# Performance work log

Measured on AMD Instinct MI355X. Metric: run time of the kernel, lower is better.

## Reference

```python
import jax, jax.numpy as jnp
import numpy as np

DIM = 256
HEADS = 8
HEAD_DIM = DIM // HEADS
WS = (2, 8, 8)  # window size (t, h, w)
N = WS[0] * WS[1] * WS[2]  # 128 tokens per window
SCALE = HEAD_DIM ** -0.5
MLP_HIDDEN = int(DIM * 2.0)
EPS = 1e-5

# static relative-position index table [N, N]
def _rel_pos_index():
    coords = np.stack(np.meshgrid(np.arange(WS[0]), np.arange(WS[1]), np.arange(WS[2]), indexing='ij'))
    cf = coords.reshape(3, -1)
    rel = cf[:, :, None] - cf[:, None, :]
    rel = rel.transpose(1, 2, 0).copy()
    rel[..., 0] += WS[0] - 1
    rel[..., 1] += WS[1] - 1
    rel[..., 2] += WS[2] - 1
    rel[..., 0] *= (2 * WS[1] - 1) * (2 * WS[2] - 1)
    rel[..., 1] *= (2 * WS[2] - 1)
    return rel.sum(-1)

REL_IDX = jnp.asarray(_rel_pos_index())  # [N, N] int
TABLE_SIZE = (2 * WS[0] - 1) * (2 * WS[1] - 1) * (2 * WS[2] - 1)  # 675


def layernorm(x, g, b):
    m = jnp.mean(x, axis=-1, keepdims=True)
    var = jnp.mean(jnp.square(x - m), axis=-1, keepdims=True)
    return (x - m) * jax.lax.rsqrt(var + EPS) * g + b


def window_partition(x):
    B, T, H, W, C = x.shape
    x = x.reshape(B, T // WS[0], WS[0], H // WS[1], WS[1], W // WS[2], WS[2], C)
    x = x.transpose(0, 1, 3, 5, 2, 4, 6, 7)
    return x.reshape(-1, N, C)


def window_reverse(wins, B, T, H, W):
    C = wins.shape[-1]
    x = wins.reshape(B, T // WS[0], H // WS[1], W // WS[2], WS[0], WS[1], WS[2], C)
    x = x.transpose(0, 1, 4, 2, 5, 3, 6, 7)
    return x.reshape(B, T, H, W, C)


def setup_inputs() -> dict:
    key = jax.random.key(0)
    ks = jax.random.split(key, 20)
    B, T, H, W = 2, 8, 64, 64
    f = lambda k, s, sc=0.02: jax.random.normal(k, s, dtype=jnp.float32) * sc
    return {
        'q': jax.random.normal(ks[0], (B, T, H, W, DIM), dtype=jnp.float32),
        'k': jax.random.normal(ks[1], (B, T, H, W, DIM), dtype=jnp.float32),
        'v': jax.random.normal(ks[2], (B, T, H, W, DIM), dtype=jnp.float32),
        'gq': jnp.ones((DIM,), jnp.float32), 'bq': jnp.zeros((DIM,), jnp.float32),
        'gk': jnp.ones((DIM,), jnp.float32), 'bk': jnp.zeros((DIM,), jnp.float32),
        'gv': jnp.ones((DIM,), jnp.float32), 'bv': jnp.zeros((DIM,), jnp.float32),
        'bias_table': f(ks[3], (TABLE_SIZE, HEADS)),
        'proj_w': f(ks[4], (DIM, DIM)), 'proj_b': jnp.zeros((DIM,), jnp.float32),
        'g2': jnp.ones((DIM,), jnp.float32), 'b2': jnp.zeros((DIM,), jnp.float32),
        'mw1': f(ks[5], (MLP_HIDDEN, DIM)), 'mb1': jnp.zeros((MLP_HIDDEN,), jnp.float32),
        'mw2': f(ks[6], (DIM, MLP_HIDDEN)), 'mb2': jnp.zeros((DIM,), jnp.float32),
    }


def reference(q, k, v, gq, bq, gk, bk, gv, bv, bias_table, proj_w, proj_b, g2, b2, mw1, mb1, mw2, mb2):
    B, T, H, W, C = q.shape
    shortcut = v
    qn = layernorm(q, gq, bq)
    kn = layernorm(k, gk, bk)
    vn = layernorm(v, gv, bv)
    # (dims divisible by window -> no padding needed)
    qw = window_partition(qn)  # [B_, N, C]
    kw = window_partition(kn)
    vw = window_partition(vn)
    B_ = qw.shape[0]
    to_heads = lambda t: t.reshape(B_, N, HEADS, HEAD_DIM).transpose(0, 2, 1, 3)  # [B_, h, N, d]
    qh, kh, vh = to_heads(qw), to_heads(kw), to_heads(vw)
    attn = jnp.einsum('bhnd,bhmd->bhnm', qh * SCALE, kh)
    bias = bias_table[REL_IDX]  # [N, N, heads]
    attn = attn + bias.transpose(2, 0, 1)[None]
    attn = jax.nn.softmax(attn, axis=-1)
    out = jnp.einsum('bhnm,bhmd->bhnd', attn, vh)
    out = out.transpose(0, 2, 1, 3).reshape(B_, N, C)
    out = out @ proj_w.T + proj_b
    x = window_reverse(out, B, T, H, W)
    x = shortcut + x
    h1 = layernorm(x, g2, b2)
    h1 = jax.nn.gelu(h1 @ mw1.T + mb1, approximate=False)
    x = x + (h1 @ mw2.T + mb2)
    return x
```

## Files before the change

kernel.cpp:

```cpp
#include <hip/hip_runtime.h>
#include <math.h>


typedef __attribute__((ext_vector_type(8))) short short8;
typedef __attribute__((ext_vector_type(4))) short shortx4;
typedef __attribute__((ext_vector_type(4))) float floatx4;

#define MFMA16(a, b, c) __builtin_amdgcn_mfma_f32_16x16x32_bf16((a), (b), (c), 0, 0, 0)
#define ATT_SCALE 0.17677669529663689f

__device__ __forceinline__ short f2bf(float f) {
  unsigned u = __float_as_uint(f);
  u += 0x7fffu + ((u >> 16) & 1u);
  return (short)(u >> 16);
}
__device__ __forceinline__ float bf2f(short s) {
  return __uint_as_float(((unsigned)(unsigned short)s) << 16);
}

__global__ void cvt_kernel(const float* __restrict__ src, short* __restrict__ dst, int n) {
  int i = blockIdx.x * 256 + threadIdx.x;
  if (i < n) dst[i] = f2bf(src[i]);
}

__global__ void biasprep_kernel(const float* __restrict__ table, short* __restrict__ biasPb) {
  int idx = blockIdx.x * 256 + threadIdx.x;
  int h = idx >> 14;
  int n = (idx >> 7) & 127;
  int lr = (idx >> 3) & 15;
  int c = idx & 7;
  int m = 16 * c + lr;
  int t1 = n >> 6, h1 = (n >> 3) & 7, w1 = n & 7;
  int t2 = m >> 6, h2 = (m >> 3) & 7, w2 = m & 7;
  int ridx = (t1 - t2 + 1) * 225 + (h1 - h2 + 7) * 15 + (w1 - w2 + 7);
  biasPb[idx] = f2bf(table[ridx * 8 + h]);
}

__global__ __launch_bounds__(256) void ln_qkv_kernel(
    const float* __restrict__ q, const float* __restrict__ k, const float* __restrict__ v,
    const float* __restrict__ gq, const float* __restrict__ bq,
    const float* __restrict__ gk, const float* __restrict__ bk,
    const float* __restrict__ gv, const float* __restrict__ bv,
    short* __restrict__ qw, short* __restrict__ kw, short* __restrict__ vw) {
  const int wv = threadIdx.x >> 6, l = threadIdx.x & 63;
  const int tok = blockIdx.x * 4 + wv;
  const int which = blockIdx.y;
  const float* src = (which == 0) ? q : ((which == 1) ? k : v);
  const float* gg  = (which == 0) ? gq : ((which == 1) ? gk : gv);
  const float* bb  = (which == 0) ? bq : ((which == 1) ? bk : bv);
  short* dst       = (which == 0) ? qw : ((which == 1) ? kw : vw);

  float4 xv = *(const float4*)(src + (size_t)tok * 256 + l * 4);
  float s1 = xv.x + xv.y + xv.z + xv.w;
  float s2 = xv.x * xv.x + xv.y * xv.y + xv.z * xv.z + xv.w * xv.w;
#pragma unroll
  for (int off = 1; off < 64; off <<= 1) {
    s1 += __shfl_xor(s1, off);
    s2 += __shfl_xor(s2, off);
  }
  float mean = s1 * (1.0f / 256.0f);
  float var = s2 * (1.0f / 256.0f) - mean * mean;
  float inv = rsqrtf(var + 1e-5f);

  int b_ = tok >> 15, rem = tok & 32767;
  int t = rem >> 12, hh = (rem >> 6) & 63, ww = rem & 63;
  int wi = ((b_ * 4 + (t >> 1)) * 8 + (hh >> 3)) * 8 + (ww >> 3);
  int n = ((t & 1) << 6) | ((hh & 7) << 3) | (ww & 7);

  float4 g4 = *(const float4*)(gg + l * 4);
  float4 b4 = *(const float4*)(bb + l * 4);
  shortx4 o;
  o[0] = f2bf((xv.x - mean) * inv * g4.x + b4.x);
  o[1] = f2bf((xv.y - mean) * inv * g4.y + b4.y);
  o[2] = f2bf((xv.z - mean) * inv * g4.z + b4.z);
  o[3] = f2bf((xv.w - mean) * inv * g4.w + b4.w);
  *(shortx4*)(dst + ((size_t)wi * 128 + n) * 256 + l * 4) = o;
}

__global__ __launch_bounds__(256, 4) void attn_kernel(
    const short* __restrict__ qw, const short* __restrict__ kw, const short* __restrict__ vw,
    const short* __restrict__ biasPb, short* __restrict__ ao) {
  __shared__ union SU {
    struct { short Qs[128][40]; short Ks[128][40]; } qk;
    short Ps[128 * 128];
  } su;
  __shared__ short Vt[32 * 128];

  const int wi = blockIdx.x, h = blockIdx.y, tid = threadIdx.x;
  const size_t base = (size_t)wi * 128 * 256 + h * 32;

#pragma unroll
  for (int i = 0; i < 2; ++i) {
    int idx = tid + 256 * i;
    int m = idx >> 2, c = idx & 3;
    *(short8*)&su.qk.Qs[m][c * 8] = *(const short8*)(qw + base + (size_t)m * 256 + c * 8);
    *(short8*)&su.qk.Ks[m][c * 8] = *(const short8*)(kw + base + (size_t)m * 256 + c * 8);
    short8 vv = *(const short8*)(vw + base + (size_t)m * 256 + c * 8);
#pragma unroll
    for (int e = 0; e < 8; ++e) {
      int d = c * 8 + e;
      Vt[d * 128 + (((m >> 3) ^ (d & 7)) << 3) + (m & 7)] = vv[e];
    }
  }
  __syncthreads();

  const int wvv = tid >> 6, l = tid & 63, lr = l & 15, g = l >> 4;
  const floatx4 zf = {0.f, 0.f, 0.f, 0.f};

  short8 aq0 = *(const short8*)&su.qk.Qs[32 * wvv + lr][g * 8];
  short8 aq1 = *(const short8*)&su.qk.Qs[32 * wvv + 16 + lr][g * 8];

  floatx4 s[2][8];
#pragma unroll
  for (int c = 0; c < 8; ++c) {
    short8 bk8 = *(const short8*)&su.qk.Ks[16 * c + lr][g * 8];
    s[0][c] = MFMA16(aq0, bk8, zf);
    s[1][c] = MFMA16(aq1, bk8, zf);
  }
  __syncthreads();

  const int lr7 = lr & 7;
#pragma unroll
  for (int r = 0; r < 2; ++r) {
#pragma unroll
    for (int j = 0; j < 4; ++j) {
      int n = 32 * wvv + 16 * r + 4 * g + j;
      short8 bv8 = *(const short8*)(biasPb + ((size_t)(h * 128 + n) * 16 + lr) * 8);
      float mx = -1e30f;
#pragma unroll
      for (int c = 0; c < 8; ++c) {
        float val = s[r][c][j] * ATT_SCALE + bf2f(bv8[c]);
        s[r][c][j] = val;
        mx = fmaxf(mx, val);
      }
#pragma unroll
      for (int off = 1; off < 16; off <<= 1) mx = fmaxf(mx, __shfl_xor(mx, off));
      float sum = 0.f;
#pragma unroll
      for (int c = 0; c < 8; ++c) {
        float e = __expf(s[r][c][j] - mx);
        s[r][c][j] = e;
        sum += e;
      }
#pragma unroll
      for (int off = 1; off < 16; off <<= 1) sum += __shfl_xor(sum, off);
      float invs = 1.0f / sum;
      int n7 = n & 7;
#pragma unroll
      for (int c = 0; c < 8; ++c) {
        int col = 16 * c + lr;
        su.Ps[n * 128 + (((col >> 3) ^ n7) << 3) + (col & 7)] = f2bf(s[r][c][j] * invs);
      }
    }
  }

  floatx4 o00 = zf, o01 = zf, o10 = zf, o11 = zf;
  const int ra0 = 32 * wvv + lr, ra1 = ra0 + 16;
#pragma unroll
  for (int ks = 0; ks < 4; ++ks) {
    int ulog = ks * 4 + g;
    short8 pa0 = *(const short8*)&su.Ps[ra0 * 128 + ((ulog ^ (ra0 & 7)) << 3)];
    short8 pa1 = *(const short8*)&su.Ps[ra1 * 128 + ((ulog ^ (ra1 & 7)) << 3)];
    short8 vb0 = *(const short8*)&Vt[lr * 128 + ((ulog ^ lr7) << 3)];
    short8 vb1 = *(const short8*)&Vt[(16 + lr) * 128 + ((ulog ^ lr7) << 3)];
    o00 = MFMA16(pa0, vb0, o00);
    o01 = MFMA16(pa0, vb1, o01);
    o10 = MFMA16(pa1, vb0, o10);
    o11 = MFMA16(pa1, vb1, o11);
  }
#pragma unroll
  for (int j = 0; j < 4; ++j) {
    int n0 = 32 * wvv + 4 * g + j;
    int n1 = n0 + 16;
    size_t rb0 = ((size_t)wi * 128 + n0) * 256 + h * 32;
    size_t rb1 = ((size_t)wi * 128 + n1) * 256 + h * 32;
    ao[rb0 + lr] = f2bf(o00[j]);
    ao[rb0 + 16 + lr] = f2bf(o01[j]);
    ao[rb1 + lr] = f2bf(o10[j]);
    ao[rb1 + 16 + lr] = f2bf(o11[j]);
  }
}

__global__ __launch_bounds__(512, 2) void projln_kernel(
    const short* __restrict__ ao, const short* __restrict__ wp,
    const float* __restrict__ proj_b, const float* __restrict__ vin,
    const float* __restrict__ g2, const float* __restrict__ b2,
    short* __restrict__ xbf, short* __restrict__ xln) {
  __shared__ short WS[256 * 256];

  const int tid = threadIdx.x;
  const int w = tid >> 6, l = tid & 63, lr = l & 15, g = l >> 4;
  const floatx4 zf = {0.f, 0.f, 0.f, 0.f};

#pragma unroll
  for (int c = 0; c < 16; ++c) {
    int idx = tid * 16 + c;
    int r = idx >> 5, u = idx & 31;
    short8 vv = *(const short8*)(wp + (size_t)r * 256 + u * 8);
    *(short8*)&WS[r * 256 + ((u ^ (r & 7)) << 3)] = vv;
  }

  const int rowbase = blockIdx.x * 256 + w * 32;
  short8 a[2][8];
#pragma unroll
  for (int mt = 0; mt < 2; ++mt)
#pragma unroll
    for (int s = 0; s < 8; ++s)
      a[mt][s] = *(const short8*)(ao + (size_t)(rowbase + mt * 16 + lr) * 256 + s * 32 + g * 8);

  __syncthreads();

  floatx4 acc[2][16];
#pragma unroll
  for (int mt = 0; mt < 2; ++mt)
#pragma unroll
    for (int ct = 0; ct < 16; ++ct) acc[mt][ct] = zf;

#pragma unroll
  for (int s = 0; s < 8; ++s) {
#pragma unroll
    for (int ct = 0; ct < 16; ++ct) {
      int rb = ct * 16 + lr;
      short8 b = *(const short8*)&WS[rb * 256 + (((s * 4 + g) ^ (rb & 7)) << 3)];
      acc[0][ct] = MFMA16(a[0][s], b, acc[0][ct]);
      acc[1][ct] = MFMA16(a[1][s], b, acc[1][ct]);
    }
  }

  float pb[16], g2v[16], b2v[16];
#pragma unroll
  for (int ct = 0; ct < 16; ++ct) {
    int col = ct * 16 + lr;
    pb[ct] = proj_b[col];
    g2v[ct] = g2[col];
    b2v[ct] = b2[col];
  }
#pragma unroll
  for (int mt = 0; mt < 2; ++mt) {
#pragma unroll
    for (int j = 0; j < 4; ++j) {
      int wrow = rowbase + mt * 16 + 4 * g + j;
      int wi = wrow >> 7, n = wrow & 127;
      int wb = wi & 7, hb = (wi >> 3) & 7, tt = (wi >> 6) & 3, b_ = wi >> 8;
      int t = tt * 2 + (n >> 6), hh = hb * 8 + ((n >> 3) & 7), ww2 = wb * 8 + (n & 7);
      size_t sidx = ((size_t)(b_ * 8 + t) * 64 + hh) * 64 + ww2;
      float xv[16], s1 = 0.f, s2 = 0.f;
#pragma unroll
      for (int ct = 0; ct < 16; ++ct) {
        float val = acc[mt][ct][j] + pb[ct] + vin[sidx * 256 + ct * 16 + lr];
        xv[ct] = val;
        s1 += val;
        s2 += val * val;
      }
#pragma unroll
      for (int off = 1; off < 16; off <<= 1) {
        s1 += __shfl_xor(s1, off);
        s2 += __shfl_xor(s2, off);
      }
      float mean = s1 * (1.0f / 256.0f);
      float var = s2 * (1.0f / 256.0f) - mean * mean;
      float inv = rsqrtf(var + 1e-5f);
#pragma unroll
      for (int ct = 0; ct < 16; ++ct) {
        int col = ct * 16 + lr;
        xbf[(size_t)wrow * 256 + col] = f2bf(xv[ct]);
        xln[(size_t)wrow * 256 + col] = f2bf((xv[ct] - mean) * inv * g2v[ct] + b2v[ct]);
      }
    }
  }
}

__global__ __launch_bounds__(512, 2) void mlp1_kernel(
    const short* __restrict__ xln, const short* __restrict__ w1,
    const float* __restrict__ mb1, short* __restrict__ h1) {
  __shared__ short WS[256 * 256];

  const int tid = threadIdx.x;
  const int w = tid >> 6, l = tid & 63, lr = l & 15, g = l >> 4;
  const int half = blockIdx.y;
  const floatx4 zf = {0.f, 0.f, 0.f, 0.f};
  const short* w1h = w1 + (size_t)half * 256 * 256;

#pragma unroll
  for (int c = 0; c < 16; ++c) {
    int idx = tid * 16 + c;
    int r = idx >> 5, u = idx & 31;
    short8 vv = *(const short8*)(w1h + (size_t)r * 256 + u * 8);
    *(short8*)&WS[r * 256 + ((u ^ (r & 7)) << 3)] = vv;
  }

  const int rowbase = blockIdx.x * 256 + w * 32;
  short8 a[2][8];
#pragma unroll
  for (int mt = 0; mt < 2; ++mt)
#pragma unroll
    for (int s = 0; s < 8; ++s)
      a[mt][s] = *(const short8*)(xln + (size_t)(rowbase + mt * 16 + lr) * 256 + s * 32 + g * 8);

  __syncthreads();

  floatx4 acc[2][16];
#pragma unroll
  for (int mt = 0; mt < 2; ++mt)
#pragma unroll
    for (int ct = 0; ct < 16; ++ct) acc[mt][ct] = zf;

#pragma unroll
  for (int s = 0; s < 8; ++s) {
#pragma unroll
    for (int ct = 0; ct < 16; ++ct) {
      int rb = ct * 16 + lr;
      short8 b = *(const short8*)&WS[rb * 256 + (((s * 4 + g) ^ (rb & 7)) << 3)];
      acc[0][ct] = MFMA16(a[0][s], b, acc[0][ct]);
      acc[1][ct] = MFMA16(a[1][s], b, acc[1][ct]);
    }
  }

  float bias[16];
#pragma unroll
  for (int ct = 0; ct < 16; ++ct) bias[ct] = mb1[half * 256 + ct * 16 + lr];
#pragma unroll
  for (int mt = 0; mt < 2; ++mt) {
#pragma unroll
    for (int j = 0; j < 4; ++j) {
      int wrow = rowbase + mt * 16 + 4 * g + j;
#pragma unroll
      for (int ct = 0; ct < 16; ++ct) {
        float xv = acc[mt][ct][j] + bias[ct];
        float yy = 1.5957691216057308f * (xv + 0.044715f * xv * xv * xv);
        float sg = 1.0f / (1.0f + __expf(-yy));
        h1[(size_t)wrow * 512 + half * 256 + ct * 16 + lr] = f2bf(xv * sg);
      }
    }
  }
}

__global__ __launch_bounds__(512, 2) void mlp2_kernel(
    const short* __restrict__ h1, const short* __restrict__ w2,
    const float* __restrict__ mb2, const short* __restrict__ xbf,
    float* __restrict__ out) {
  __shared__ short WS[128 * 512];

  const int tid = threadIdx.x;
  const int w = tid >> 6, l = tid & 63, lr = l & 15, g = l >> 4;
  const int half = blockIdx.y;
  const floatx4 zf = {0.f, 0.f, 0.f, 0.f};
  const short* w2h = w2 + (size_t)half * 128 * 512;

#pragma unroll
  for (int c = 0; c < 16; ++c) {
    int idx = tid * 16 + c;
    int r = idx >> 6, u = idx & 63;
    short8 vv = *(const short8*)(w2h + (size_t)r * 512 + u * 8);
    *(short8*)&WS[r * 512 + ((u ^ (r & 7)) << 3)] = vv;
  }
  __syncthreads();

  const int rowbase = blockIdx.x * 256 + w * 32;
  floatx4 acc[2][8];
#pragma unroll
  for (int mt = 0; mt < 2; ++mt)
#pragma unroll
    for (int ct = 0; ct < 8; ++ct) acc[mt][ct] = zf;

#pragma unroll
  for (int hk = 0; hk < 2; ++hk) {
    short8 a[2][8];
#pragma unroll
    for (int mt = 0; mt < 2; ++mt)
#pragma unroll
      for (int s = 0; s < 8; ++s)
        a[mt][s] = *(const short8*)(h1 + (size_t)(rowbase + mt * 16 + lr) * 512 +
                                    hk * 256 + s * 32 + g * 8);
#pragma unroll
    for (int s = 0; s < 8; ++s) {
      int S = hk * 8 + s;
#pragma unroll
      for (int ct = 0; ct < 8; ++ct) {
        int rb = ct * 16 + lr;
        short8 b = *(const short8*)&WS[rb * 512 + (((S * 4 + g) ^ (rb & 7)) << 3)];
        acc[0][ct] = MFMA16(a[0][s], b, acc[0][ct]);
        acc[1][ct] = MFMA16(a[1][s], b, acc[1][ct]);
      }
    }
  }

  float bias[8];
#pragma unroll
  for (int ct = 0; ct < 8; ++ct) bias[ct] = mb2[half * 128 + ct * 16 + lr];
#pragma unroll
  for (int mt = 0; mt < 2; ++mt) {
#pragma unroll
    for (int j = 0; j < 4; ++j) {
      int wrow = rowbase + mt * 16 + 4 * g + j;
      int wi = wrow >> 7, n = wrow & 127;
      int wb = wi & 7, hb = (wi >> 3) & 7, tt = (wi >> 6) & 3, b_ = wi >> 8;
      int t = tt * 2 + (n >> 6), hh = hb * 8 + ((n >> 3) & 7), ww2 = wb * 8 + (n & 7);
      size_t sidx = ((size_t)(b_ * 8 + t) * 64 + hh) * 64 + ww2;
#pragma unroll
      for (int ct = 0; ct < 8; ++ct) {
        int col = half * 128 + ct * 16 + lr;
        out[sidx * 256 + col] =
            bf2f(xbf[(size_t)wrow * 256 + col]) + acc[mt][ct][j] + bias[ct];
      }
    }
  }
}

extern "C" void kernel_launch(void* const* d_in, const int* in_sizes, int n_in,
                              void* d_out, int out_size, void* d_ws, size_t ws_size,
                              hipStream_t stream) {
  const float* q = (const float*)d_in[0];
  const float* k = (const float*)d_in[1];
  const float* v = (const float*)d_in[2];
  const float* gq = (const float*)d_in[3];
  const float* bq = (const float*)d_in[4];
  const float* gk = (const float*)d_in[5];
  const float* bk = (const float*)d_in[6];
  const float* gv = (const float*)d_in[7];
  const float* bv = (const float*)d_in[8];
  const float* bias_table = (const float*)d_in[9];
  const float* proj_w = (const float*)d_in[10];
  const float* proj_b = (const float*)d_in[11];
  const float* g2 = (const float*)d_in[12];
  const float* b2 = (const float*)d_in[13];
  const float* mw1 = (const float*)d_in[14];
  const float* mb1 = (const float*)d_in[15];
  const float* mw2 = (const float*)d_in[16];
  const float* mb2 = (const float*)d_in[17];

  char* ws = (char*)d_ws;
  short* qw = (short*)(ws + 0);
  short* kw = (short*)(ws + 33554432);
  short* vw = (short*)(ws + 67108864);
  short* ao = (short*)(ws + 100663296);
  short* xln = (short*)(ws + 0);
  short* xbf = (short*)(ws + 33554432);
  short* h1 = (short*)(ws + 67108864);
  short* wp = (short*)(ws + 167772160);
  short* w1 = (short*)(ws + 167903232);
  short* w2 = (short*)(ws + 168165376);
  short* biasPb = (short*)(ws + 168427520);

  cvt_kernel<<<256, 256, 0, stream>>>(proj_w, wp, 65536);
  cvt_kernel<<<512, 256, 0, stream>>>(mw1, w1, 131072);
  cvt_kernel<<<512, 256, 0, stream>>>(mw2, w2, 131072);
  biasprep_kernel<<<512, 256, 0, stream>>>(bias_table, biasPb);

  ln_qkv_kernel<<<dim3(16384, 3), 256, 0, stream>>>(q, k, v, gq, bq, gk, bk, gv, bv, qw, kw, vw);

  attn_kernel<<<dim3(512, 8), 256, 0, stream>>>(qw, kw, vw, biasPb, ao);

  projln_kernel<<<256, 512, 0, stream>>>(ao, wp, proj_b, v, g2, b2, xbf, xln);

  mlp1_kernel<<<dim3(256, 2), 512, 0, stream>>>(xln, w1, mb1, h1);

  mlp2_kernel<<<dim3(256, 2), 512, 0, stream>>>(h1, w2, mb2, xbf, (float*)d_out);
}
```

Before: 256.5 us.

## Write attention output in spatial order and transpose MFMA operands for vectorized epilogues

The attention kernel now scatters its output directly into spatial (B,T,H,W) token order, so the projection and MLP kernels index tokens linearly instead of recomputing window-reverse addresses. The three GEMM kernels swap MFMA operands so each lane holds four consecutive output columns for one token, which allows float4 and short4 vector loads and stores in the epilogues. They also stage weights into LDS in two K-halves, halving shared memory, and launch twice as many 128-row blocks with higher occupancy bounds. The cost is scattered writes in the attention epilogue, an extra barrier per GEMM, and weight tiles reloaded by more blocks.

```diff
diff --git a/kernel.cpp b/kernel.cpp
--- a/kernel.cpp
+++ b/kernel.cpp
@@ -168,12 +168,15 @@
     o10 = MFMA16(pa1, vb0, o10);
     o11 = MFMA16(pa1, vb1, o11);
   }
+  const int wbx = wi & 7, hbx = (wi >> 3) & 7, ttx = (wi >> 6) & 3, bbx = wi >> 8;
 #pragma unroll
   for (int j = 0; j < 4; ++j) {
     int n0 = 32 * wvv + 4 * g + j;
     int n1 = n0 + 16;
-    size_t rb0 = ((size_t)wi * 128 + n0) * 256 + h * 32;
-    size_t rb1 = ((size_t)wi * 128 + n1) * 256 + h * 32;
+    int t0 = ttx * 2 + (n0 >> 6), hh0 = hbx * 8 + ((n0 >> 3) & 7), ww0 = wbx * 8 + (n0 & 7);
+    int t1 = ttx * 2 + (n1 >> 6), hh1 = hbx * 8 + ((n1 >> 3) & 7), ww1 = wbx * 8 + (n1 & 7);
+    size_t rb0 = (((size_t)(bbx * 8 + t0) * 64 + hh0) * 64 + ww0) * 256 + h * 32;
+    size_t rb1 = (((size_t)(bbx * 8 + t1) * 64 + hh1) * 64 + ww1) * 256 + h * 32;
     ao[rb0 + lr] = f2bf(o00[j]);
     ao[rb0 + 16 + lr] = f2bf(o01[j]);
     ao[rb1 + lr] = f2bf(o10[j]);
@@ -181,229 +184,191 @@
   }
 }
 
-__global__ __launch_bounds__(512, 2) void projln_kernel(
+__global__ __launch_bounds__(512, 4) void projln_kernel(
     const short* __restrict__ ao, const short* __restrict__ wp,
     const float* __restrict__ proj_b, const float* __restrict__ vin,
     const float* __restrict__ g2, const float* __restrict__ b2,
     short* __restrict__ xbf, short* __restrict__ xln) {
-  __shared__ short WS[256 * 256];
+  __shared__ short WS[256 * 128];
 
   const int tid = threadIdx.x;
   const int w = tid >> 6, l = tid & 63, lr = l & 15, g = l >> 4;
   const floatx4 zf = {0.f, 0.f, 0.f, 0.f};
-
-#pragma unroll
-  for (int c = 0; c < 16; ++c) {
-    int idx = tid * 16 + c;
-    int r = idx >> 5, u = idx & 31;
-    short8 vv = *(const short8*)(wp + (size_t)r * 256 + u * 8);
-    *(short8*)&WS[r * 256 + ((u ^ (r & 7)) << 3)] = vv;
-  }
-
-  const int rowbase = blockIdx.x * 256 + w * 32;
-  short8 a[2][8];
-#pragma unroll
-  for (int mt = 0; mt < 2; ++mt)
-#pragma unroll
-    for (int s = 0; s < 8; ++s)
-      a[mt][s] = *(const short8*)(ao + (size_t)(rowbase + mt * 16 + lr) * 256 + s * 32 + g * 8);
-
-  __syncthreads();
-
-  floatx4 acc[2][16];
-#pragma unroll
-  for (int mt = 0; mt < 2; ++mt)
-#pragma unroll
-    for (int ct = 0; ct < 16; ++ct) acc[mt][ct] = zf;
-
-#pragma unroll
-  for (int s = 0; s < 8; ++s) {
-#pragma unroll
-    for (int ct = 0; ct < 16; ++ct) {
-      int rb = ct * 16 + lr;
-      short8 b = *(const short8*)&WS[rb * 256 + (((s * 4 + g) ^ (rb & 7)) << 3)];
-      acc[0][ct] = MFMA16(a[0][s], b, acc[0][ct]);
-      acc[1][ct] = MFMA16(a[1][s], b, acc[1][ct]);
-    }
-  }
-
-  float pb[16], g2v[16], b2v[16];
+  const size_t token = (size_t)blockIdx.x * 128 + w * 16 + lr;
+
+  floatx4 acc[16];
+#pragma unroll
+  for (int i = 0; i < 16; ++i) acc[i] = zf;
+
+#pragma unroll
+  for (int ph = 0; ph < 2; ++ph) {
+    if (ph) __syncthreads();
+#pragma unroll
+    for (int c = 0; c < 8; ++c) {
+      int idx = tid * 8 + c;
+      int r = idx >> 4, u = idx & 15;
+      short8 vv = *(const short8*)(wp + (size_t)r * 256 + ph * 128 + u * 8);
+      *(short8*)&WS[r * 128 + ((u ^ (r & 7)) << 3)] = vv;
+    }
+    __syncthreads();
+    short8 a[4];
+#pragma unroll
+    for (int s = 0; s < 4; ++s)
+      a[s] = *(const short8*)(ao + token * 256 + ph * 128 + s * 32 + g * 8);
+#pragma unroll
+    for (int s = 0; s < 4; ++s) {
+#pragma unroll
+      for (int ct = 0; ct < 16; ++ct) {
+        int rb = ct * 16 + lr;
+        short8 wf = *(const short8*)&WS[rb * 128 + (((s * 4 + g) ^ (rb & 7)) << 3)];
+        acc[ct] = MFMA16(wf, a[s], acc[ct]);
+      }
+    }
+  }
+
+  float s1 = 0.f, s2 = 0.f;
 #pragma unroll
   for (int ct = 0; ct < 16; ++ct) {
-    int col = ct * 16 + lr;
-    pb[ct] = proj_b[col];
-    g2v[ct] = g2[col];
-    b2v[ct] = b2[col];
-  }
-#pragma unroll
-  for (int mt = 0; mt < 2; ++mt) {
+    float4 pb = *(const float4*)(proj_b + ct * 16 + 4 * g);
+    float4 vv = *(const float4*)(vin + token * 256 + ct * 16 + 4 * g);
 #pragma unroll
     for (int j = 0; j < 4; ++j) {
-      int wrow = rowbase + mt * 16 + 4 * g + j;
-      int wi = wrow >> 7, n = wrow & 127;
-      int wb = wi & 7, hb = (wi >> 3) & 7, tt = (wi >> 6) & 3, b_ = wi >> 8;
-      int t = tt * 2 + (n >> 6), hh = hb * 8 + ((n >> 3) & 7), ww2 = wb * 8 + (n & 7);
-      size_t sidx = ((size_t)(b_ * 8 + t) * 64 + hh) * 64 + ww2;
-      float xv[16], s1 = 0.f, s2 = 0.f;
-#pragma unroll
-      for (int ct = 0; ct < 16; ++ct) {
-        float val = acc[mt][ct][j] + pb[ct] + vin[sidx * 256 + ct * 16 + lr];
-        xv[ct] = val;
-        s1 += val;
-        s2 += val * val;
-      }
-#pragma unroll
-      for (int off = 1; off < 16; off <<= 1) {
-        s1 += __shfl_xor(s1, off);
-        s2 += __shfl_xor(s2, off);
-      }
-      float mean = s1 * (1.0f / 256.0f);
-      float var = s2 * (1.0f / 256.0f) - mean * mean;
-      float inv = rsqrtf(var + 1e-5f);
-#pragma unroll
-      for (int ct = 0; ct < 16; ++ct) {
-        int col = ct * 16 + lr;
-        xbf[(size_t)wrow * 256 + col] = f2bf(xv[ct]);
-        xln[(size_t)wrow * 256 + col] = f2bf((xv[ct] - mean) * inv * g2v[ct] + b2v[ct]);
-      }
-    }
-  }
-}
-
-__global__ __launch_bounds__(512, 2) void mlp1_kernel(
+      float val = acc[ct][j] + ((const float*)&pb)[j] + ((const float*)&vv)[j];
+      acc[ct][j] = val;
+      s1 += val;
+      s2 += val * val;
+    }
+  }
+  s1 += __shfl_xor(s1, 16); s1 += __shfl_xor(s1, 32);
+  s2 += __shfl_xor(s2, 16); s2 += __shfl_xor(s2, 32);
+  float mean = s1 * (1.0f / 256.0f);
+  float var = s2 * (1.0f / 256.0f) - mean * mean;
+  float inv = rsqrtf(var + 1e-5f);
+#pragma unroll
+  for (int ct = 0; ct < 16; ++ct) {
+    float4 gg = *(const float4*)(g2 + ct * 16 + 4 * g);
+    float4 bb = *(const float4*)(b2 + ct * 16 + 4 * g);
+    shortx4 xo, lo;
+#pragma unroll
+    for (int j = 0; j < 4; ++j) {
+      xo[j] = f2bf(acc[ct][j]);
+      lo[j] = f2bf((acc[ct][j] - mean) * inv * ((const float*)&gg)[j] + ((const float*)&bb)[j]);
+    }
+    *(shortx4*)(xbf + token * 256 + ct * 16 + 4 * g) = xo;
+    *(shortx4*)(xln + token * 256 + ct * 16 + 4 * g) = lo;
+  }
+}
+
+__global__ __launch_bounds__(512, 4) void mlp1_kernel(
     const short* __restrict__ xln, const short* __restrict__ w1,
     const float* __restrict__ mb1, short* __restrict__ h1) {
-  __shared__ short WS[256 * 256];
+  __shared__ short WS[256 * 128];
 
   const int tid = threadIdx.x;
   const int w = tid >> 6, l = tid & 63, lr = l & 15, g = l >> 4;
   const int half = blockIdx.y;
   const floatx4 zf = {0.f, 0.f, 0.f, 0.f};
   const short* w1h = w1 + (size_t)half * 256 * 256;
-
-#pragma unroll
-  for (int c = 0; c < 16; ++c) {
-    int idx = tid * 16 + c;
-    int r = idx >> 5, u = idx & 31;
-    short8 vv = *(const short8*)(w1h + (size_t)r * 256 + u * 8);
-    *(short8*)&WS[r * 256 + ((u ^ (r & 7)) << 3)] = vv;
-  }
-
-  const int rowbase = blockIdx.x * 256 + w * 32;
-  short8 a[2][8];
-#pragma unroll
-  for (int mt = 0; mt < 2; ++mt)
-#pragma unroll
-    for (int s = 0; s < 8; ++s)
-      a[mt][s] = *(const short8*)(xln + (size_t)(rowbase + mt * 16 + lr) * 256 + s * 32 + g * 8);
-
-  __syncthreads();
-
-  floatx4 acc[2][16];
-#pragma unroll
-  for (int mt = 0; mt < 2; ++mt)
-#pragma unroll
-    for (int ct = 0; ct < 16; ++ct) acc[mt][ct] = zf;
-
-#pragma unroll
-  for (int s = 0; s < 8; ++s) {
-#pragma unroll
-    for (int ct = 0; ct < 16; ++ct) {
-      int rb = ct * 16 + lr;
-      short8 b = *(const short8*)&WS[rb * 256 + (((s * 4 + g) ^ (rb & 7)) << 3)];
-      acc[0][ct] = MFMA16(a[0][s], b, acc[0][ct]);
-      acc[1][ct] = MFMA16(a[1][s], b, acc[1][ct]);
-    }
-  }
-
-  float bias[16];
-#pragma unroll
-  for (int ct = 0; ct < 16; ++ct) bias[ct] = mb1[half * 256 + ct * 16 + lr];
-#pragma unroll
-  for (int mt = 0; mt < 2; ++mt) {
+  const size_t token = (size_t)blockIdx.x * 128 + w * 16 + lr;
+
+  floatx4 acc[16];
+#pragma unroll
+  for (int i = 0; i < 16; ++i) acc[i] = zf;
+
+#pragma unroll
+  for (int ph = 0; ph < 2; ++ph) {
+    if (ph) __syncthreads();
+#pragma unroll
+    for (int c = 0; c < 8; ++c) {
+      int idx = tid * 8 + c;
+      int r = idx >> 4, u = idx & 15;
+      short8 vv = *(const short8*)(w1h + (size_t)r * 256 + ph * 128 + u * 8);
+      *(short8*)&WS[r * 128 + ((u ^ (r & 7)) << 3)] = vv;
+    }
+    __syncthreads();
+    short8 a[4];
+#pragma unroll
+    for (int s = 0; s < 4; ++s)
+      a[s] = *(const short8*)(xln + token * 256 + ph * 128 + s * 32 + g * 8);
+#pragma unroll
+    for (int s = 0; s < 4; ++s) {
+#pragma unroll
+      for (int ct = 0; ct < 16; ++ct) {
+        int rb = ct * 16 + lr;
+        short8 wf = *(const short8*)&WS[rb * 128 + (((s * 4 + g) ^ (rb & 7)) << 3)];
+        acc[ct] = MFMA16(wf, a[s], acc[ct]);
+      }
+    }
+  }
+
+#pragma unroll
+  for (int ct = 0; ct < 16; ++ct) {
+    float4 bb = *(const float4*)(mb1 + half * 256 + ct * 16 + 4 * g);
+    shortx4 ho;
 #pragma unroll
     for (int j = 0; j < 4; ++j) {
-      int wrow = rowbase + mt * 16 + 4 * g + j;
-#pragma unroll
-      for (int ct = 0; ct < 16; ++ct) {
-        float xv = acc[mt][ct][j] + bias[ct];
-        float yy = 1.5957691216057308f * (xv + 0.044715f * xv * xv * xv);
-        float sg = 1.0f / (1.0f + __expf(-yy));
-        h1[(size_t)wrow * 512 + half * 256 + ct * 16 + lr] = f2bf(xv * sg);
-      }
-    }
-  }
-}
-
-__global__ __launch_bounds__(512, 2) void mlp2_kernel(
+      float xv = acc[ct][j] + ((const float*)&bb)[j];
+      float yy = 1.5957691216057308f * (xv + 0.044715f * xv * xv * xv);
+      float sg = 1.0f / (1.0f + __expf(-yy));
+      ho[j] = f2bf(xv * sg);
+    }
+    *(shortx4*)(h1 + token * 512 + half * 256 + ct * 16 + 4 * g) = ho;
+  }
+}
+
+__global__ __launch_bounds__(512, 4) void mlp2_kernel(
     const short* __restrict__ h1, const short* __restrict__ w2,
     const float* __restrict__ mb2, const short* __restrict__ xbf,
     float* __restrict__ out) {
-  __shared__ short WS[128 * 512];
+  __shared__ short WS[128 * 256];
 
   const int tid = threadIdx.x;
   const int w = tid >> 6, l = tid & 63, lr = l & 15, g = l >> 4;
   const int half = blockIdx.y;
   const floatx4 zf = {0.f, 0.f, 0.f, 0.f};
   const short* w2h = w2 + (size_t)half * 128 * 512;
-
-#pragma unroll
-  for (int c = 0; c < 16; ++c) {
-    int idx = tid * 16 + c;
-    int r = idx >> 6, u = idx & 63;
-    short8 vv = *(const short8*)(w2h + (size_t)r * 512 + u * 8);
-    *(short8*)&WS[r * 512 + ((u ^ (r & 7)) << 3)] = vv;
-  }
-  __syncthreads();
-
-  const int rowbase = blockIdx.x * 256 + w * 32;
-  floatx4 acc[2][8];
-#pragma unroll
-  for (int mt = 0; mt < 2; ++mt)
-#pragma unroll
-    for (int ct = 0; ct < 8; ++ct) acc[mt][ct] = zf;
-
-#pragma unroll
-  for (int hk = 0; hk < 2; ++hk) {
-    short8 a[2][8];
-#pragma unroll
-    for (int mt = 0; mt < 2; ++mt)
-#pragma unroll
-      for (int s = 0; s < 8; ++s)
-        a[mt][s] = *(const short8*)(h1 + (size_t)(rowbase + mt * 16 + lr) * 512 +
-                                    hk * 256 + s * 32 + g * 8);
+  const size_t token = (size_t)blockIdx.x * 128 + w * 16 + lr;
+
+  floatx4 acc[8];
+#pragma unroll
+  for (int i = 0; i < 8; ++i) acc[i] = zf;
+
+#pragma unroll
+  for (int ph = 0; ph < 2; ++ph) {
+    if (ph) __syncthreads();
+#pragma unroll
+    for (int c = 0; c < 8; ++c) {
+      int idx = tid * 8 + c;
+      int r = idx >> 5, u = idx & 31;
+      short8 vv = *(const short8*)(w2h + (size_t)r * 512 + ph * 256 + u * 8);
+      *(short8*)&WS[r * 256 + ((u ^ (r & 7)) << 3)] = vv;
+    }
+    __syncthreads();
+    short8 a[8];
+#pragma unroll
+    for (int s = 0; s < 8; ++s)
+      a[s] = *(const short8*)(h1 + token * 512 + ph * 256 + s * 32 + g * 8);
 #pragma unroll
     for (int s = 0; s < 8; ++s) {
-      int S = hk * 8 + s;
 #pragma unroll
       for (int ct = 0; ct < 8; ++ct) {
         int rb = ct * 16 + lr;
-        short8 b = *(const short8*)&WS[rb * 512 + (((S * 4 + g) ^ (rb & 7)) << 3)];
-        acc[0][ct] = MFMA16(a[0][s], b, acc[0][ct]);
-        acc[1][ct] = MFMA16(a[1][s], b, acc[1][ct]);
-      }
-    }
-  }
-
-  float bias[8];
-#pragma unroll
-  for (int ct = 0; ct < 8; ++ct) bias[ct] = mb2[half * 128 + ct * 16 + lr];
-#pragma unroll
-  for (int mt = 0; mt < 2; ++mt) {
-#pragma unroll
-    for (int j = 0; j < 4; ++j) {
-      int wrow = rowbase + mt * 16 + 4 * g + j;
-      int wi = wrow >> 7, n = wrow & 127;
-      int wb = wi & 7, hb = (wi >> 3) & 7, tt = (wi >> 6) & 3, b_ = wi >> 8;
-      int t = tt * 2 + (n >> 6), hh = hb * 8 + ((n >> 3) & 7), ww2 = wb * 8 + (n & 7);
-      size_t sidx = ((size_t)(b_ * 8 + t) * 64 + hh) * 64 + ww2;
-#pragma unroll
-      for (int ct = 0; ct < 8; ++ct) {
-        int col = half * 128 + ct * 16 + lr;
-        out[sidx * 256 + col] =
-            bf2f(xbf[(size_t)wrow * 256 + col]) + acc[mt][ct][j] + bias[ct];
-      }
-    }
+        short8 wf = *(const short8*)&WS[rb * 256 + (((s * 4 + g) ^ (rb & 7)) << 3)];
+        acc[ct] = MFMA16(wf, a[s], acc[ct]);
+      }
+    }
+  }
+
+#pragma unroll
+  for (int ct = 0; ct < 8; ++ct) {
+    int oc = half * 128 + ct * 16 + 4 * g;
+    float4 bb = *(const float4*)(mb2 + oc);
+    shortx4 xb = *(const shortx4*)(xbf + token * 256 + oc);
+    float4 o;
+#pragma unroll
+    for (int j = 0; j < 4; ++j)
+      ((float*)&o)[j] = bf2f(xb[j]) + acc[ct][j] + ((const float*)&bb)[j];
+    *(float4*)(out + token * 256 + oc) = o;
   }
 }
 
@@ -451,9 +416,9 @@
 
   attn_kernel<<<dim3(512, 8), 256, 0, stream>>>(qw, kw, vw, biasPb, ao);
 
-  projln_kernel<<<256, 512, 0, stream>>>(ao, wp, proj_b, v, g2, b2, xbf, xln);
-
-  mlp1_kernel<<<dim3(256, 2), 512, 0, stream>>>(xln, w1, mb1, h1);
-
-  mlp2_kernel<<<dim3(256, 2), 512, 0, stream>>>(h1, w2, mb2, xbf, (float*)d_out);
-}
+  projln_kernel<<<512, 512, 0, stream>>>(ao, wp, proj_b, v, g2, b2, xbf, xln);
+
+  mlp1_kernel<<<dim3(512, 2), 512, 0, stream>>>(xln, w1, mb1, h1);
+
+  mlp2_kernel<<<dim3(512, 2), 512, 0, stream>>>(h1, w2, mb2, xbf, (float*)d_out);
+}
```

New measurement: 293.6 us. 14.5% more time.
